# Optimization experiments

Hardware: AMD Instinct MI355X
Metric: run time of the kernel (lower is better)

The kernel has to match this reference:

```python
import jax, jax.numpy as jnp
import numpy as np

DIM_X = 256
DIM_V = 512
DIM_IN = 2
N = 65536
EPS = 0.05          # posdef_tol
CRLB = 0.0          # contraction_rate_lb
STD = 0.5           # weight_init_std


def setup_inputs() -> dict:
    key = jax.random.key(0)
    ks = jax.random.split(key, 8)
    return {
        "t": 0,
        "x": jax.random.normal(ks[0], (N, DIM_X), jnp.float32),
        "Pstar": jax.random.normal(ks[1], (DIM_X, DIM_X), jnp.float32) * STD,
        "Chi": jax.random.normal(ks[2], (DIM_X, DIM_V), jnp.float32) * STD,
        "X": jax.random.normal(ks[3], (DIM_X + DIM_V, DIM_X + DIM_V), jnp.float32) * STD,
        "Y1": jax.random.normal(ks[4], (DIM_X, DIM_X), jnp.float32) * STD,
        "B2": jax.random.normal(ks[5], (DIM_X, DIM_IN), jnp.float32) * STD,
        "D12": jax.random.normal(ks[6], (DIM_V, DIM_IN), jnp.float32) * STD,
        "bv": jnp.zeros((DIM_V,), jnp.float32),
        "bx": jnp.zeros((DIM_X,), jnp.float32),
    }


def _model_matrices(Pstar, Chi, X, Y1):
    """Replicates CREN.update_model_param (F.linear(a,b) == a @ b.T)."""
    dx = Pstar.shape[0]
    P = 0.5 * (Pstar @ Pstar.T) + EPS * jnp.eye(dx, dtype=Pstar.dtype)
    H = X @ X.T + EPS * jnp.eye(X.shape[0], dtype=X.dtype)
    H1 = H[:dx, :dx]
    H2 = H[:dx, dx:]
    H4 = H[dx:, dx:]
    Y = -0.5 * (H1 + CRLB * P + Y1 - Y1.T)
    lam = 0.5 * jnp.diagonal(H4)                 # Lambda is diagonal
    Pinv = jnp.linalg.inv(P)
    A = Pinv @ Y                                  # F.linear(inv(P), Y.T)
    D11 = -jnp.tril(H4, -1) / lam[:, None]        # strictly lower triangular
    C1 = Chi.T / lam[:, None]                     # (dv, dx)
    B1 = Pinv @ (-H2 - Chi)                       # (dx, dv)
    return A, B1, C1, D11


def reference(t, x, Pstar, Chi, X, Y1, B2, D12, bv, bx):
    A, B1, C1, D11 = _model_matrices(Pstar, Chi, X, Y1)
    n = x.shape[0]
    u = jnp.zeros((1, DIM_IN), x.dtype)           # hard-coded zero input in forward
    # precompute the per-step linear terms that do not depend on w:
    # cx[:, i] == F.linear(x, C1[i]) + bv[i] + F.linear(u, D12[i])
    cx = x @ C1.T + bv[None, :] + u @ D12.T       # (n, dv)

    idx = jnp.arange(DIM_V)

    def step(w, xs):
        i, cxi, d_row = xs                        # cxi: (n,), d_row: (dv,)
        v = cxi + w @ d_row                       # forward substitution step
        w = w.at[:, i].set(jnp.tanh(v))
        return w, None

    w0 = jnp.zeros((n, DIM_V), x.dtype)
    w, _ = jax.lax.scan(step, w0, (idx, cx.T, D11))

    x_dot = x @ A.T + w @ B1.T + bx[None, :] + u @ B2.T
    return x_dot


if __name__ == "__main__":
    out = reference(**setup_inputs())
    print(out.shape, out.dtype)
```

## Files before the change

kernel.cpp:

```cpp
#include <hip/hip_runtime.h>
#include <cstdint>
#include <cstddef>

#define DIMX 256
#define DIMV 512
#define DIMH 768
#define EPSV 0.05f

typedef __bf16 bf16x8 __attribute__((ext_vector_type(8)));
typedef unsigned short u16x8 __attribute__((ext_vector_type(8)));
typedef unsigned int u32x4 __attribute__((ext_vector_type(4)));
typedef float f32x4 __attribute__((ext_vector_type(4)));

__device__ __forceinline__ unsigned short f2bf(float f) {
  unsigned int u = __float_as_uint(f);
  u += 0x7fffu + ((u >> 16) & 1u);
  return (unsigned short)(u >> 16);
}
__device__ __forceinline__ float bf2f(unsigned short b) {
  return __uint_as_float(((unsigned int)b) << 16);
}
__device__ __forceinline__ bf16x8 ld8(const unsigned short* p) {
  u16x8 u = *reinterpret_cast<const u16x8*>(p);
  return __builtin_bit_cast(bf16x8, u);
}
__device__ __forceinline__ f32x4 mfma16(bf16x8 a, bf16x8 b, f32x4 c) {
  return __builtin_amdgcn_mfma_f32_16x16x32_bf16(a, b, c, 0, 0, 0);
}
__device__ __forceinline__ float rdlane(float v, int lane) {
  return __uint_as_float(
      (unsigned int)__builtin_amdgcn_readlane((int)__float_as_uint(v), lane));
}

__global__ __launch_bounds__(256) void k_setup1(const float* __restrict__ X,
                                                unsigned short* __restrict__ Xhi,
                                                unsigned short* __restrict__ Xlo,
                                                const float* __restrict__ Pst,
                                                float* __restrict__ P) {
  int blk = blockIdx.x;
  if (blk < 256) {
    int bi = blk >> 4, bj = blk & 15;
    int ty = threadIdx.x >> 4, tx = threadIdx.x & 15;
    int i = bi * 16 + ty, j = bj * 16 + tx;
    const f32x4* ra = reinterpret_cast<const f32x4*>(Pst + (size_t)i * DIMX);
    const f32x4* rb = reinterpret_cast<const f32x4*>(Pst + (size_t)j * DIMX);
    float s = 0.f;
    for (int k = 0; k < 64; ++k) {
      f32x4 a = ra[k], b = rb[k];
      s = fmaf(a[0], b[0], s); s = fmaf(a[1], b[1], s);
      s = fmaf(a[2], b[2], s); s = fmaf(a[3], b[3], s);
    }
    P[(size_t)i * DIMX + j] = 0.5f * s + (i == j ? EPSV : 0.f);
  } else {
    int idx = (blk - 256) * 256 + threadIdx.x;
    if (idx < DIMH * DIMH) {
      float f = X[idx];
      unsigned short h = f2bf(f);
      Xhi[idx] = h;
      Xlo[idx] = f2bf(f - bf2f(h));
    }
  }
}

__global__ __launch_bounds__(256, 1) void k_setup2(float* __restrict__ A,
                                                   float* __restrict__ Li,
                                                   const unsigned short* __restrict__ Xhi,
                                                   const unsigned short* __restrict__ Xlo,
                                                   float* __restrict__ H) {
  __shared__ float Wl[32][33];
  __shared__ float T[32][232];
  __shared__ float Lp2[224][33];
  if (blockIdx.x == 0) {
    int t = threadIdx.x;
    int wv = t >> 6, l = t & 63;
#pragma unroll 1
    for (int s = 0; s < 8; ++s) {
      int K = 32 * s;
      int R32 = 256 - K - 32;
      if (wv == 0) {
        int li = l & 31;
        float d[32];
#pragma unroll
        for (int j = 0; j < 32; ++j) d[j] = A[(K + j) * 256 + K + li];
#pragma unroll
        for (int k = 0; k < 32; ++k) {
          float dkk = rdlane(d[k], k);
          float ip = rsqrtf(dkk);
          d[k] *= ip;
#pragma unroll
          for (int j = k + 1; j < 32; ++j) {
            float ljk = rdlane(d[k], j);
            d[j] = fmaf(-ljk, d[k], d[j]);
          }
        }
        float wcol[32];
#pragma unroll
        for (int i = 0; i < 32; ++i) {
          float Lii = rdlane(d[i], i);
          float ipi = 1.0f / Lii;
          float acc = (li == i) ? 1.0f : 0.0f;
#pragma unroll
          for (int k = 0; k < i; ++k) {
            float Lik = rdlane(d[k], i);
            acc = fmaf(-Lik, wcol[k], acc);
          }
          wcol[i] = acc * ipi;
        }
        if (l < 32) {
#pragma unroll
          for (int k = 0; k < 32; ++k) {
            Wl[k][l] = wcol[k];
            Li[(32 * s + k) * 256 + 32 * s + l] = wcol[k];
          }
        }
      }
      __syncthreads();
      if (R32 > 0) {
        int nrt = R32 >> 2;
        for (int u = t; u < nrt * 8; u += 256) {
          int rt = u >> 3, jg = u & 7;
          int r = K + 32 + rt * 4;
          int j0 = jg * 4;
          f32x4 z4 = {0.f, 0.f, 0.f, 0.f};
          f32x4 acc[4] = {z4, z4, z4, z4};
#pragma unroll
          for (int k = 0; k < 32; ++k) {
            f32x4 av = *reinterpret_cast<const f32x4*>(&A[(K + k) * 256 + r]);
#pragma unroll
            for (int jj = 0; jj < 4; ++jj) {
              float w = Wl[j0 + jj][k];
              acc[jj][0] = fmaf(av[0], w, acc[jj][0]);
              acc[jj][1] = fmaf(av[1], w, acc[jj][1]);
              acc[jj][2] = fmaf(av[2], w, acc[jj][2]);
              acc[jj][3] = fmaf(av[3], w, acc[jj][3]);
            }
          }
#pragma unroll
          for (int jj = 0; jj < 4; ++jj)
            *reinterpret_cast<f32x4*>(&T[j0 + jj][rt * 4]) = acc[jj];
        }
        __syncthreads();
#pragma unroll 1
        for (int j = 0; j < 32; ++j) {
          int rl = t << 2;
          if (rl < R32)
            *reinterpret_cast<f32x4*>(&A[(K + j) * 256 + K + 32 + rl]) =
                *reinterpret_cast<const f32x4*>(&T[j][rl]);
        }
        int T4 = R32 >> 2;
        int ntile = T4 * (T4 + 1) / 2;
        for (int idx = t; idx < ntile; idx += 256) {
          int ti = (int)((sqrtf(8.0f * (float)idx + 1.0f) - 1.0f) * 0.5f);
          while ((ti + 1) * (ti + 2) / 2 <= idx) ++ti;
          while (ti * (ti + 1) / 2 > idx) --ti;
          int tj = idx - ti * (ti + 1) / 2;
          int gi = K + 32 + 4 * ti, gj = K + 32 + 4 * tj;
          f32x4 acc[4];
#pragma unroll
          for (int jj = 0; jj < 4; ++jj)
            acc[jj] = *reinterpret_cast<const f32x4*>(&A[(gj + jj) * 256 + gi]);
#pragma unroll
          for (int k = 0; k < 32; ++k) {
            f32x4 av = *reinterpret_cast<const f32x4*>(&T[k][4 * ti]);
            f32x4 bv = *reinterpret_cast<const f32x4*>(&T[k][4 * tj]);
#pragma unroll
            for (int jj = 0; jj < 4; ++jj) {
              acc[jj][0] = fmaf(-av[0], bv[jj], acc[jj][0]);
              acc[jj][1] = fmaf(-av[1], bv[jj], acc[jj][1]);
              acc[jj][2] = fmaf(-av[2], bv[jj], acc[jj][2]);
              acc[jj][3] = fmaf(-av[3], bv[jj], acc[jj][3]);
            }
          }
#pragma unroll
          for (int jj = 0; jj < 4; ++jj)
            *reinterpret_cast<f32x4*>(&A[(gj + jj) * 256 + gi]) = acc[jj];
        }
      }
      __syncthreads();
    }

    float* Tb = &T[0][0];
#pragma unroll 1
    for (int i = 1; i < 8; ++i) {
      for (int idx = t; idx < 32 * 32 * i; idx += 256) {
        int r = idx & 31, cc = idx >> 5;
        Lp2[cc][r] = A[cc * 256 + 32 * i + r];
      }
      for (int idx = t; idx < 1024; idx += 256) {
        int r = idx >> 5, kk = idx & 31;
        Wl[r][kk] = Li[(32 * i + r) * 256 + 32 * i + kk];
      }
      __syncthreads();
      int nt1 = i * 64;
      for (int u = t; u < nt1; u += 256) {
        int j = u >> 6, v = u & 63;
        int r0 = (v >> 3) * 4, c0 = (v & 7) * 4;
        f32x4 z4 = {0.f, 0.f, 0.f, 0.f};
        f32x4 acc[4] = {z4, z4, z4, z4};
        for (int k = j; k < i; ++k) {
#pragma unroll
          for (int kk = 0; kk < 32; ++kk) {
            f32x4 lv = *reinterpret_cast<const f32x4*>(
                &Li[(32 * k + kk) * 256 + 32 * j + c0]);
#pragma unroll
            for (int e = 0; e < 4; ++e) {
              float lpe = Lp2[32 * k + kk][r0 + e];
              acc[e][0] = fmaf(lpe, lv[0], acc[e][0]);
              acc[e][1] = fmaf(lpe, lv[1], acc[e][1]);
              acc[e][2] = fmaf(lpe, lv[2], acc[e][2]);
              acc[e][3] = fmaf(lpe, lv[3], acc[e][3]);
            }
          }
        }
#pragma unroll
        for (int e = 0; e < 4; ++e)
          *reinterpret_cast<f32x4*>(&Tb[j * 1024 + (r0 + e) * 32 + c0]) = acc[e];
      }
      __syncthreads();
      for (int u = t; u < nt1; u += 256) {
        int j = u >> 6, v = u & 63;
        int r0 = (v >> 3) * 4, c0 = (v & 7) * 4;
        f32x4 z4 = {0.f, 0.f, 0.f, 0.f};
        f32x4 acc[4] = {z4, z4, z4, z4};
#pragma unroll
        for (int kk = 0; kk < 32; ++kk) {
          f32x4 tv = *reinterpret_cast<const f32x4*>(&Tb[j * 1024 + kk * 32 + c0]);
#pragma unroll
          for (int e = 0; e < 4; ++e) {
            float w = Wl[r0 + e][kk];
            acc[e][0] = fmaf(-w, tv[0], acc[e][0]);
            acc[e][1] = fmaf(-w, tv[1], acc[e][1]);
            acc[e][2] = fmaf(-w, tv[2], acc[e][2]);
            acc[e][3] = fmaf(-w, tv[3], acc[e][3]);
          }
        }
#pragma unroll
        for (int e = 0; e < 4; ++e)
          *reinterpret_cast<f32x4*>(&Li[(32 * i + r0 + e) * 256 + 32 * j + c0]) =
              acc[e];
      }
      __syncthreads();
    }
  } else {
    int b2 = blockIdx.x - 1;
    int bx = b2 % 12, by = b2 / 12;
    int i0 = by * 64, j0 = bx * 64;
    int l = threadIdx.x & 63, wv = threadIdx.x >> 6;
    int lr = l & 15, lq = l >> 4;
    int koff = lq * 8;
    int arow = i0 + wv * 16 + lr;
    f32x4 z = {0.f, 0.f, 0.f, 0.f};
    f32x4 acc[4] = {z, z, z, z};
    for (int pass = 0; pass < 3; ++pass) {
      const unsigned short* Xa = (pass == 2) ? Xlo : Xhi;
      const unsigned short* Xb = (pass == 1) ? Xlo : Xhi;
      for (int kc = 0; kc < 24; ++kc) {
        bf16x8 a = ld8(&Xa[(size_t)arow * DIMH + kc * 32 + koff]);
#pragma unroll
        for (int ct = 0; ct < 4; ++ct) {
          bf16x8 b = ld8(&Xb[(size_t)(j0 + ct * 16 + lr) * DIMH + kc * 32 + koff]);
          acc[ct] = mfma16(a, b, acc[ct]);
        }
      }
    }
#pragma unroll
    for (int ct = 0; ct < 4; ++ct)
#pragma unroll
      for (int r = 0; r < 4; ++r) {
        int i = i0 + wv * 16 + lq * 4 + r;
        int j = j0 + ct * 16 + lr;
        H[(size_t)i * DIMH + j] = acc[ct][r] + (i == j ? EPSV : 0.f);
      }
  }
}

__global__ __launch_bounds__(256, 2) void k_setup3(const float* __restrict__ H,
                                                   const float* __restrict__ Chi,
                                                   unsigned short* __restrict__ Gin,
                                                   const float* __restrict__ Li,
                                                   float* __restrict__ Pinv) {
  int blk = blockIdx.x;
  int t = threadIdx.x;
  if (blk < 36) {
    int bi = (int)((sqrtf(8.0f * (float)blk + 1.0f) - 1.0f) * 0.5f);
    while ((bi + 1) * (bi + 2) / 2 <= blk) ++bi;
    while (bi * (bi + 1) / 2 > blk) --bi;
    int bj = blk - bi * (bi + 1) / 2;
    int r = t >> 3, c0 = (t & 7) * 4;
    f32x4 acc = {0.f, 0.f, 0.f, 0.f};
    for (int kb = bi; kb < 8; ++kb) {
#pragma unroll
      for (int kk = 0; kk < 32; ++kk) {
        float a = Li[(32 * kb + kk) * 256 + 32 * bi + r];
        f32x4 b = *reinterpret_cast<const f32x4*>(
            &Li[(32 * kb + kk) * 256 + 32 * bj + c0]);
        acc[0] = fmaf(a, b[0], acc[0]);
        acc[1] = fmaf(a, b[1], acc[1]);
        acc[2] = fmaf(a, b[2], acc[2]);
        acc[3] = fmaf(a, b[3], acc[3]);
      }
    }
    *reinterpret_cast<f32x4*>(&Pinv[(32 * bi + r) * 256 + 32 * bj + c0]) = acc;
    if (bi != bj) {
#pragma unroll
      for (int e = 0; e < 4; ++e)
        Pinv[(32 * bj + c0 + e) * 256 + 32 * bi + r] = acc[e];
    }
    return;
  }
  int b2 = blk - 36;
  int xb = b2 % 3, c = b2 / 3;
  int q = xb * 256 + t;
  float rlam = 2.f / H[(size_t)(256 + c) * DIMH + 256 + c];
  float v;
  if (q < 256) {
    v = Chi[(size_t)q * DIMV + c] * rlam;
  } else {
    int j = q - 256;
    v = (j < c) ? -H[(size_t)(256 + c) * DIMH + 256 + j] * rlam : 0.f;
  }
  Gin[(size_t)c * DIMH + q] = f2bf(v);
}

__global__ __launch_bounds__(256) void k_gout(const float* __restrict__ Pinv,
                                              const float* __restrict__ H,
                                              const float* __restrict__ Y1,
                                              const float* __restrict__ Chi,
                                              unsigned short* __restrict__ Gout) {
  __shared__ float Ps[32][33], Bs[32][33];
  int q0 = blockIdx.x * 32, i0 = blockIdx.y * 32;
  int t = threadIdx.x;
  int tx = t & 31, ty = t >> 5;
  int lrr = t >> 3, lc4 = (t & 7) * 4;
  float acc[4] = {0.f, 0.f, 0.f, 0.f};
  for (int kc = 0; kc < 8; ++kc) {
    int k0 = kc * 32;
    f32x4 pv = *reinterpret_cast<const f32x4*>(&Pinv[(size_t)(i0 + lrr) * 256 + k0 + lc4]);
    Ps[lrr][lc4 + 0] = pv[0]; Ps[lrr][lc4 + 1] = pv[1];
    Ps[lrr][lc4 + 2] = pv[2]; Ps[lrr][lc4 + 3] = pv[3];
    int k = k0 + lrr;
#pragma unroll
    for (int e = 0; e < 4; ++e) {
      int q = q0 + lc4 + e;
      float v;
      if (q < 256) {
        v = -0.5f * (H[(size_t)k * DIMH + q] + Y1[(size_t)k * 256 + q] - Y1[(size_t)q * 256 + k]);
      } else {
        int c = q - 256;
        v = -(H[(size_t)k * DIMH + 256 + c] + Chi[(size_t)k * DIMV + c]);
      }
      Bs[lrr][lc4 + e] = v;
    }
    __syncthreads();
#pragma unroll
    for (int kk = 0; kk < 32; ++kk) {
      float bb = Bs[kk][tx];
#pragma unroll
      for (int rr = 0; rr < 4; ++rr) acc[rr] = fmaf(Ps[4 * ty + rr][kk], bb, acc[rr]);
    }
    __syncthreads();
  }
#pragma unroll
  for (int rr = 0; rr < 4; ++rr)
    Gout[(size_t)(i0 + 4 * ty + rr) * DIMH + q0 + tx] = f2bf(acc[rr]);
}

#define ACCSTR 33
#define ACC_W 4224
#define DD_W 2048
#define WT_W 2560
#define SMEM_MAIN (4 * (ACC_W + DD_W + WT_W))

__global__ __launch_bounds__(256, 2) void k_main(const float* __restrict__ x,
                                                 const unsigned short* __restrict__ Gin,
                                                 const unsigned short* __restrict__ Gout,
                                                 const float* __restrict__ bv,
                                                 const float* __restrict__ bx,
                                                 float* __restrict__ out) {
  extern __shared__ char smem[];
  int tid = threadIdx.x;
  int wv = tid >> 6, l = tid & 63;
  int lr = l & 15, lq = l >> 4, koff = lq * 8;
  float* accb = (float*)(smem + wv * ACC_W);
  char* ddiag = smem + 4 * ACC_W + wv * DD_W;
  char* wtmp = smem + 4 * ACC_W + 4 * DD_W + wv * WT_W;

  int rowbase = blockIdx.x * 128 + wv * 32;

  bf16x8 frag0[24], frag1[24];
  {
    u16x8 zz = {0, 0, 0, 0, 0, 0, 0, 0};
#pragma unroll
    for (int c = 8; c < 24; ++c) {
      frag0[c] = __builtin_bit_cast(bf16x8, zz);
      frag1[c] = __builtin_bit_cast(bf16x8, zz);
    }
  }
#pragma unroll
  for (int kc = 0; kc < 8; ++kc) {
    const float* xr0 = x + (size_t)(rowbase + lr) * 256 + koff + kc * 32;
    const float* xr1 = x + (size_t)(rowbase + 16 + lr) * 256 + koff + kc * 32;
    f32x4 a0 = *reinterpret_cast<const f32x4*>(xr0);
    f32x4 a1 = *reinterpret_cast<const f32x4*>(xr0 + 4);
    f32x4 b0 = *reinterpret_cast<const f32x4*>(xr1);
    f32x4 b1 = *reinterpret_cast<const f32x4*>(xr1 + 4);
    u16x8 u0, u1;
#pragma unroll
    for (int e = 0; e < 4; ++e) {
      u0[e] = f2bf(a0[e]); u0[4 + e] = f2bf(a1[e]);
      u1[e] = f2bf(b0[e]); u1[4 + e] = f2bf(b1[e]);
    }
    frag0[kc] = __builtin_bit_cast(bf16x8, u0);
    frag1[kc] = __builtin_bit_cast(bf16x8, u1);
  }

  f32x4 z = {0.f, 0.f, 0.f, 0.f};

#pragma unroll 1
  for (int b = 0; b < 16; ++b) {
#pragma unroll
    for (int t = 0; t < 2; ++t) {
      int row = t * 16 + (l >> 2);
      const unsigned short* src =
          Gin + (size_t)(32 * b + row) * DIMH + 256 + 32 * b + (l & 3) * 8;
      u16x8 v = *reinterpret_cast<const u16x8*>(src);
      *reinterpret_cast<u16x8*>(ddiag + t * 1024 + l * 16) = v;
    }

    f32x4 a00 = z, a01 = z, a10 = z, a11 = z;
    const unsigned short* gb0 = Gin + (size_t)(32 * b + lr) * DIMH + koff;
    const unsigned short* gb1 = gb0 + 16 * DIMH;
#pragma unroll
    for (int g = 0; g < 6; ++g) {
      if (g * 4 < 8 + b) {
#pragma unroll
        for (int cc = 0; cc < 4; ++cc) {
          int c = g * 4 + cc;
          bf16x8 bb0 = ld8(gb0 + c * 32);
          bf16x8 bb1 = ld8(gb1 + c * 32);
          a00 = mfma16(frag0[c], bb0, a00);
          a01 = mfma16(frag0[c], bb1, a01);
          a10 = mfma16(frag1[c], bb0, a10);
          a11 = mfma16(frag1[c], bb1, a11);
        }
      }
    }

    float bv0 = bv[32 * b + lr], bv1 = bv[32 * b + 16 + lr];
#pragma unroll
    for (int r = 0; r < 4; ++r) {
      accb[(lq * 4 + r) * ACCSTR + lr] = a00[r] + bv0;
      accb[(lq * 4 + r) * ACCSTR + 16 + lr] = a01[r] + bv1;
      accb[(16 + lq * 4 + r) * ACCSTR + lr] = a10[r] + bv0;
      accb[(16 + lq * 4 + r) * ACCSTR + 16 + lr] = a11[r] + bv1;
    }

    if (l < 32) {
      const unsigned int* dd = (const unsigned int*)ddiag;
      unsigned int* wrow = (unsigned int*)(wtmp + l * 80);
      float wf[32];
      unsigned int cur = 0;
#pragma unroll
      for (int i = 0; i < 32; ++i) {
        float p0 = 0.f, p1 = 0.f;
        const unsigned int* ddr = dd + i * 16;
#pragma unroll
        for (int j = 0; j < i; ++j) {
          unsigned int pw = ddr[j >> 1];
          float dj = __uint_as_float((j & 1) ? (pw & 0xffff0000u) : (pw << 16));
          if (j & 1) p1 = fmaf(dj, wf[j], p1);
          else       p0 = fmaf(dj, wf[j], p0);
        }
        float s = accb[l * ACCSTR + i] + p0 + p1;
        float e = __builtin_amdgcn_exp2f(s * 2.885390082f);
        float w = fmaf(-2.f, __builtin_amdgcn_rcpf(e + 1.f), 1.f);
        wf[i] = w;
        unsigned int hb = (unsigned int)f2bf(w);
        if (i & 1) { cur |= hb << 16; wrow[i >> 1] = cur; }
        else       cur = hb;
      }
    }

    bf16x8 nw0 = ld8((const unsigned short*)(wtmp + lr * 80 + lq * 16));
    bf16x8 nw1 = ld8((const unsigned short*)(wtmp + (16 + lr) * 80 + lq * 16));
#pragma unroll
    for (int j = 0; j < 16; ++j) {
      if (b == j) { frag0[8 + j] = nw0; frag1[8 + j] = nw1; }
    }
  }

#pragma unroll 1
  for (int ct = 0; ct < 16; ++ct) {
    f32x4 o0 = z, o1 = z;
    const unsigned short* gg = Gout + (size_t)(ct * 16 + lr) * DIMH + koff;
#pragma unroll
    for (int c = 0; c < 24; ++c) {
      bf16x8 bb = ld8(gg + c * 32);
      o0 = mfma16(frag0[c], bb, o0);
      o1 = mfma16(frag1[c], bb, o1);
    }
    float bxv = bx[ct * 16 + lr];
#pragma unroll
    for (int r = 0; r < 4; ++r) {
      out[(size_t)(rowbase + lq * 4 + r) * 256 + ct * 16 + lr] = o0[r] + bxv;
      out[(size_t)(rowbase + 16 + lq * 4 + r) * 256 + ct * 16 + lr] = o1[r] + bxv;
    }
  }
}

extern "C" void kernel_launch(void* const* d_in, const int* in_sizes, int n_in,
                              void* d_out, int out_size, void* d_ws, size_t ws_size,
                              hipStream_t stream) {
  const float* x   = (const float*)d_in[1];
  const float* Pst = (const float*)d_in[2];
  const float* Chi = (const float*)d_in[3];
  const float* X   = (const float*)d_in[4];
  const float* Y1  = (const float*)d_in[5];
  const float* bv  = (const float*)d_in[8];
  const float* bx  = (const float*)d_in[9];
  float* out = (float*)d_out;

  char* ws = (char*)d_ws;
  const size_t OFF_H    = 0;
  const size_t OFF_P    = 2359296;
  const size_t OFF_XHI  = 2883584;
  const size_t OFF_XLO  = 4063232;
  const size_t OFF_GIN  = 5242880;
  const size_t OFF_GOUT = 6029312;
  if (ws_size < 6422528) return;

  float* H    = (float*)(ws + OFF_H);
  float* P    = (float*)(ws + OFF_P);
  float* Li   = (float*)(ws + OFF_GOUT);
  unsigned short* Xhi  = (unsigned short*)(ws + OFF_XHI);
  unsigned short* Xlo  = (unsigned short*)(ws + OFF_XLO);
  unsigned short* Gin  = (unsigned short*)(ws + OFF_GIN);
  unsigned short* Gout = (unsigned short*)(ws + OFF_GOUT);

  k_setup1<<<2560, 256, 0, stream>>>(X, Xhi, Xlo, Pst, P);
  k_setup2<<<145, 256, 0, stream>>>(P, Li, Xhi, Xlo, H);
  k_setup3<<<1572, 256, 0, stream>>>(H, Chi, Gin, Li, P);
  dim3 go(24, 8);
  k_gout<<<go, 256, 0, stream>>>(P, H, Y1, Chi, Gout);
  k_main<<<512, 256, SMEM_MAIN, stream>>>(x, Gin, Gout, bv, bx, out);
}
```

Measured before the change: 606.3 us.

## Widen Cholesky setup block to 1024 threads and drop Lp2 staging

The single-block Cholesky/triangular-inverse stage in k_setup2 now runs with 1024 threads instead of 256, spreading its tile loops across more waves. The Lp2 shared-memory staging copy is removed, and L panel values are read directly from global memory as float4. The diagonal-block inverse now reads L from a shared-memory tile (Ld) instead of doing cross-lane reads. The other 144 GEMM blocks launch 1024 threads but return early for threads past 256, which wastes launch slots and may reduce occupancy.

```diff
diff --git a/kernel.cpp b/kernel.cpp
--- a/kernel.cpp
+++ b/kernel.cpp
@@ -62,16 +62,16 @@
   }
 }
 
-__global__ __launch_bounds__(256, 1) void k_setup2(float* __restrict__ A,
-                                                   float* __restrict__ Li,
-                                                   const unsigned short* __restrict__ Xhi,
-                                                   const unsigned short* __restrict__ Xlo,
-                                                   float* __restrict__ H) {
+__global__ __launch_bounds__(1024, 1) void k_setup2(float* __restrict__ A,
+                                                    float* __restrict__ Li,
+                                                    const unsigned short* __restrict__ Xhi,
+                                                    const unsigned short* __restrict__ Xlo,
+                                                    float* __restrict__ H) {
+  __shared__ float Ld[32][33];
   __shared__ float Wl[32][33];
   __shared__ float T[32][232];
-  __shared__ float Lp2[224][33];
+  int t = threadIdx.x;
   if (blockIdx.x == 0) {
-    int t = threadIdx.x;
     int wv = t >> 6, l = t & 63;
 #pragma unroll 1
     for (int s = 0; s < 8; ++s) {
@@ -79,45 +79,53 @@
       int R32 = 256 - K - 32;
       if (wv == 0) {
         int li = l & 31;
-        float d[32];
-#pragma unroll
-        for (int j = 0; j < 32; ++j) d[j] = A[(K + j) * 256 + K + li];
-#pragma unroll
-        for (int k = 0; k < 32; ++k) {
-          float dkk = rdlane(d[k], k);
-          float ip = rsqrtf(dkk);
-          d[k] *= ip;
-#pragma unroll
-          for (int j = k + 1; j < 32; ++j) {
-            float ljk = rdlane(d[k], j);
-            d[j] = fmaf(-ljk, d[k], d[j]);
-          }
-        }
-        float wcol[32];
-#pragma unroll
-        for (int i = 0; i < 32; ++i) {
-          float Lii = rdlane(d[i], i);
-          float ipi = 1.0f / Lii;
-          float acc = (li == i) ? 1.0f : 0.0f;
-#pragma unroll
-          for (int k = 0; k < i; ++k) {
-            float Lik = rdlane(d[k], i);
-            acc = fmaf(-Lik, wcol[k], acc);
-          }
-          wcol[i] = acc * ipi;
-        }
-        if (l < 32) {
+        {
+          float d[32];
+#pragma unroll
+          for (int j = 0; j < 32; ++j) d[j] = A[(K + j) * 256 + K + li];
 #pragma unroll
           for (int k = 0; k < 32; ++k) {
-            Wl[k][l] = wcol[k];
-            Li[(32 * s + k) * 256 + 32 * s + l] = wcol[k];
+            float dkk = rdlane(d[k], k);
+            float ip = rsqrtf(dkk);
+            d[k] *= ip;
+#pragma unroll
+            for (int j = k + 1; j < 32; ++j) {
+              float ljk = rdlane(d[k], j);
+              d[j] = fmaf(-ljk, d[k], d[j]);
+            }
+          }
+          if (l < 32) {
+#pragma unroll
+            for (int j = 0; j < 32; ++j) Ld[li][j] = d[j];
+          }
+        }
+        {
+          float wcol[32];
+#pragma unroll
+          for (int i = 0; i < 32; ++i) {
+            float Lii = Ld[i][i];
+            float ipi = 1.0f / Lii;
+            float acc = (li == i) ? 1.0f : 0.0f;
+#pragma unroll
+            for (int k = 0; k < i; ++k) {
+              float Lik = Ld[i][k];
+              acc = fmaf(-Lik, wcol[k], acc);
+            }
+            wcol[i] = acc * ipi;
+          }
+          if (l < 32) {
+#pragma unroll
+            for (int k = 0; k < 32; ++k) {
+              Wl[k][l] = wcol[k];
+              Li[(32 * s + k) * 256 + 32 * s + l] = wcol[k];
+            }
           }
         }
       }
       __syncthreads();
       if (R32 > 0) {
         int nrt = R32 >> 2;
-        for (int u = t; u < nrt * 8; u += 256) {
+        for (int u = t; u < nrt * 8; u += 1024) {
           int rt = u >> 3, jg = u & 7;
           int r = K + 32 + rt * 4;
           int j0 = jg * 4;
@@ -140,16 +148,18 @@
             *reinterpret_cast<f32x4*>(&T[j0 + jj][rt * 4]) = acc[jj];
         }
         __syncthreads();
+        {
+          int rl = t << 2;
+          if (rl < R32) {
 #pragma unroll 1
-        for (int j = 0; j < 32; ++j) {
-          int rl = t << 2;
-          if (rl < R32)
-            *reinterpret_cast<f32x4*>(&A[(K + j) * 256 + K + 32 + rl]) =
-                *reinterpret_cast<const f32x4*>(&T[j][rl]);
+            for (int j = 0; j < 32; ++j)
+              *reinterpret_cast<f32x4*>(&A[(K + j) * 256 + K + 32 + rl]) =
+                  *reinterpret_cast<const f32x4*>(&T[j][rl]);
+          }
         }
         int T4 = R32 >> 2;
         int ntile = T4 * (T4 + 1) / 2;
-        for (int idx = t; idx < ntile; idx += 256) {
+        for (int idx = t; idx < ntile; idx += 1024) {
           int ti = (int)((sqrtf(8.0f * (float)idx + 1.0f) - 1.0f) * 0.5f);
           while ((ti + 1) * (ti + 2) / 2 <= idx) ++ti;
           while (ti * (ti + 1) / 2 > idx) --ti;
@@ -182,17 +192,13 @@
     float* Tb = &T[0][0];
 #pragma unroll 1
     for (int i = 1; i < 8; ++i) {
-      for (int idx = t; idx < 32 * 32 * i; idx += 256) {
-        int r = idx & 31, cc = idx >> 5;
-        Lp2[cc][r] = A[cc * 256 + 32 * i + r];
-      }
-      for (int idx = t; idx < 1024; idx += 256) {
-        int r = idx >> 5, kk = idx & 31;
+      if (t < 1024) {
+        int r = t >> 5, kk = t & 31;
         Wl[r][kk] = Li[(32 * i + r) * 256 + 32 * i + kk];
       }
       __syncthreads();
       int nt1 = i * 64;
-      for (int u = t; u < nt1; u += 256) {
+      for (int u = t; u < nt1; u += 1024) {
         int j = u >> 6, v = u & 63;
         int r0 = (v >> 3) * 4, c0 = (v & 7) * 4;
         f32x4 z4 = {0.f, 0.f, 0.f, 0.f};
@@ -200,15 +206,16 @@
         for (int k = j; k < i; ++k) {
 #pragma unroll
           for (int kk = 0; kk < 32; ++kk) {
+            f32x4 lp = *reinterpret_cast<const f32x4*>(
+                &A[(32 * k + kk) * 256 + 32 * i + r0]);
             f32x4 lv = *reinterpret_cast<const f32x4*>(
                 &Li[(32 * k + kk) * 256 + 32 * j + c0]);
 #pragma unroll
             for (int e = 0; e < 4; ++e) {
-              float lpe = Lp2[32 * k + kk][r0 + e];
-              acc[e][0] = fmaf(lpe, lv[0], acc[e][0]);
-              acc[e][1] = fmaf(lpe, lv[1], acc[e][1]);
-              acc[e][2] = fmaf(lpe, lv[2], acc[e][2]);
-              acc[e][3] = fmaf(lpe, lv[3], acc[e][3]);
+              acc[e][0] = fmaf(lp[e], lv[0], acc[e][0]);
+              acc[e][1] = fmaf(lp[e], lv[1], acc[e][1]);
+              acc[e][2] = fmaf(lp[e], lv[2], acc[e][2]);
+              acc[e][3] = fmaf(lp[e], lv[3], acc[e][3]);
             }
           }
         }
@@ -217,7 +224,7 @@
           *reinterpret_cast<f32x4*>(&Tb[j * 1024 + (r0 + e) * 32 + c0]) = acc[e];
       }
       __syncthreads();
-      for (int u = t; u < nt1; u += 256) {
+      for (int u = t; u < nt1; u += 1024) {
         int j = u >> 6, v = u & 63;
         int r0 = (v >> 3) * 4, c0 = (v & 7) * 4;
         f32x4 z4 = {0.f, 0.f, 0.f, 0.f};
@@ -242,10 +249,11 @@
       __syncthreads();
     }
   } else {
+    if (t >= 256) return;
     int b2 = blockIdx.x - 1;
     int bx = b2 % 12, by = b2 / 12;
     int i0 = by * 64, j0 = bx * 64;
-    int l = threadIdx.x & 63, wv = threadIdx.x >> 6;
+    int l = t & 63, wv = t >> 6;
     int lr = l & 15, lq = l >> 4;
     int koff = lq * 8;
     int arow = i0 + wv * 16 + lr;
@@ -538,7 +546,7 @@
   unsigned short* Gout = (unsigned short*)(ws + OFF_GOUT);
 
   k_setup1<<<2560, 256, 0, stream>>>(X, Xhi, Xlo, Pst, P);
-  k_setup2<<<145, 256, 0, stream>>>(P, Li, Xhi, Xlo, H);
+  k_setup2<<<145, 1024, 0, stream>>>(P, Li, Xhi, Xlo, H);
   k_setup3<<<1572, 256, 0, stream>>>(H, Chi, Gin, Li, P);
   dim3 go(24, 8);
   k_gout<<<go, 256, 0, stream>>>(P, H, Y1, Chi, Gout);
```

Result: slower. 900.0 us (+48.5%).
